# Kernel optimization log

Measured on AMD Instinct MI355X. Metric: run time of the kernel, lower is better.

The kernel has to match this reference:

```python
import jax, jax.numpy as jnp
import numpy as np

IN_F = 256
OUT_F = 64
ALPHA = 0.2  # LeakyReLU negative slope
MASK_VAL = -9e15


def _glorot(key, shape):
    r = np.sqrt(6.0 / (shape[0] + shape[1]))
    return jax.random.uniform(key, shape, jnp.float32, -r, r)


def setup_inputs() -> dict:
    key = jax.random.key(0)
    k_h, k_adj, k_W, k_a = jax.random.split(key, 4)
    B, N = 4, 4096
    h = jax.random.normal(k_h, (B, N, IN_F), jnp.float32)
    adj = jax.random.randint(k_adj, (B, N, N), 0, 2, jnp.int32)
    W = _glorot(k_W, (IN_F, OUT_F))
    a = _glorot(k_a, (2 * OUT_F, 1))
    bias = jnp.zeros((OUT_F,), jnp.float32)
    return {"h": h, "adj": adj, "W": W, "a": a, "bias": bias}


def reference(h, adj, W, a, bias):
    # Wh: [B, N, F_out]
    Wh = jnp.matmul(h, W) + bias
    # additive attention: e_ij = leakyrelu(Wh_i . a1 + Wh_j . a2)
    Wh1 = jnp.matmul(Wh, a[:OUT_F, :])   # [B, N, 1]
    Wh2 = jnp.matmul(Wh, a[OUT_F:, :])   # [B, N, 1]
    e = Wh1 + jnp.swapaxes(Wh2, 2, 1)    # [B, N, N]
    e = jnp.where(e > 0, e, ALPHA * e)   # LeakyReLU
    e = jnp.where(adj > 0, e, MASK_VAL)
    attention = jax.nn.softmax(e, axis=2)
    h_prime = jnp.matmul(attention, Wh)  # [B, N, F_out]
    return jax.nn.elu(h_prime)           # concat=True -> ELU
```

## Files before the change

### kernel.cpp

```cpp
#include <hip/hip_runtime.h>
#include <hip/hip_bf16.h>
#include <cstdint>

#define IN_F 256
#define OUT_F 64
#define NB 4
#define NN 4096
#define ALPHA 0.2f
#define LOG2E 1.4426950408889634f

typedef __attribute__((ext_vector_type(4))) float f32x4;
typedef __attribute__((ext_vector_type(4))) int i32x4;
typedef __attribute__((ext_vector_type(8))) short bf16x8;

static __device__ __forceinline__ ushort f2bf(float x) {
  uint32_t u = __float_as_uint(x);
  uint32_t r = (u + 0x7fffu + ((u >> 16) & 1u)) >> 16;
  return (ushort)r;
}

static __device__ __forceinline__ void gl16(const void* g, void* l) {
  __builtin_amdgcn_global_load_lds(
      (const __attribute__((address_space(1))) void*)g,
      (__attribute__((address_space(3))) void*)l, 16, 0, 0);
}
#define FENCE() asm volatile("" ::: "memory")

__global__ __launch_bounds__(256) void k1_gemm(
    const float* __restrict__ h, const float* __restrict__ W,
    const float* __restrict__ a, const float* __restrict__ bias,
    ushort* __restrict__ WhT, float* __restrict__ Wh1, float* __restrict__ Wh2)
{
  __shared__ float hs[32][33];
  __shared__ float Ws[32][64];
  const int t  = threadIdx.x;
  const int tx = t & 15;
  const int ty = t >> 4;
  const int row0 = blockIdx.x * 32;

  float acc[2][4] = {};

  for (int k0 = 0; k0 < IN_F; k0 += 32) {
    {
      int r = t >> 3, c4 = t & 7;
      *(f32x4*)&hs[r][c4 * 4] =
          *(const f32x4*)(h + (size_t)(row0 + r) * IN_F + k0 + c4 * 4);
    }
    #pragma unroll
    for (int s = 0; s < 2; ++s) {
      int f4 = t + 256 * s;
      int kk = f4 >> 4, c4 = f4 & 15;
      *(f32x4*)&Ws[kk][c4 * 4] = *(const f32x4*)(W + (size_t)(k0 + kk) * OUT_F + c4 * 4);
    }
    __syncthreads();
    #pragma unroll 8
    for (int kk = 0; kk < 32; ++kk) {
      f32x4 bv = *(const f32x4*)&Ws[kk][tx * 4];
      float av0 = hs[ty * 2 + 0][kk];
      float av1 = hs[ty * 2 + 1][kk];
      #pragma unroll
      for (int j = 0; j < 4; ++j) {
        acc[0][j] += av0 * bv[j];
        acc[1][j] += av1 * bv[j];
      }
    }
    __syncthreads();
  }

  #pragma unroll
  for (int i = 0; i < 2; ++i) {
    int row = row0 + ty * 2 + i;
    float s1 = 0.f, s2 = 0.f;
    #pragma unroll
    for (int j = 0; j < 4; ++j) {
      float v = acc[i][j] + bias[tx * 4 + j];
      acc[i][j] = v;
      s1 += v * a[tx * 4 + j];
      s2 += v * a[64 + tx * 4 + j];
    }
    #pragma unroll
    for (int off = 1; off < 16; off <<= 1) {
      s1 += __shfl_xor(s1, off);
      s2 += __shfl_xor(s2, off);
    }
    if (tx == 0) { Wh1[row] = s1 * LOG2E; Wh2[row] = s2 * LOG2E; }
    int bb = row >> 12;
    int n  = row & 4095;
    #pragma unroll
    for (int j = 0; j < 4; ++j) {
      WhT[(((size_t)(bb * OUT_F + tx * 4 + j)) << 12) + n] = f2bf(acc[i][j]);
    }
  }
}

#define NDEPTH 5
#define ADJ_BUF 16384
#define WHT_OFF 81920
#define WHT_BUF 8192
#define WH2_OFF 122880
#define LDS_TOTAL 139264
__global__ __launch_bounds__(512, 1) void k2_attn(
    const int* __restrict__ adj, const ushort* __restrict__ WhT,
    const float* __restrict__ Wh1, const float* __restrict__ Wh2,
    float* __restrict__ out)
{
  extern __shared__ char smem[];
  const int t  = threadIdx.x;
  const int l  = t & 63;
  const int w  = t >> 6;
  const int rq = w >> 1;
  const int kq = w & 1;
  const int g  = l >> 4;
  const int lr = l & 15;
  const int b  = blockIdx.y;
  const int r0 = blockIdx.x << 6;

  const int   rowl = rq * 16 + lr;
  const float wh1  = Wh1[(b << 12) + r0 + rowl];
  asm volatile("" :: "v"(wh1));

  const int*    adjb = adj + ((size_t)b << 24) + ((size_t)r0 << 12);
  const ushort* whb  = WhT + ((size_t)(b * OUT_F) << 12);

  const int*    srcA[4]; int ldsA[4];
  const ushort* srcW[2]; int ldsW[2];
  if (w < 4) {
    #pragma unroll
    for (int i = 0; i < 4; ++i) {
      int e   = ((w * 4 + i) << 6) + l;
      int row = e >> 4;
      int ch  = (e & 15) ^ (row & 7);
      srcA[i] = adjb + (size_t)row * 4096 + (ch << 2);
      ldsA[i] = e << 4;
    }
  } else {
    #pragma unroll
    for (int i = 0; i < 2; ++i) {
      int e    = (((w - 4) * 2 + i) << 6) + l;
      int feat = e >> 3;
      int ch   = (e & 7) ^ (feat & 7);
      srcW[i] = whb + ((size_t)feat << 12) + (ch << 3);
      ldsW[i] = e << 4;
    }
  }

  auto STAGE_A = [&](int s) {
    char* base = smem + (s % NDEPTH) * ADJ_BUF;
    #pragma unroll
    for (int i = 0; i < 4; ++i) gl16(srcA[i] + (s << 6), base + ldsA[i]);
  };
  auto STAGE_W = [&](int s) {
    char* base = smem + WHT_OFF + (s % NDEPTH) * WHT_BUF;
    #pragma unroll
    for (int i = 0; i < 2; ++i) gl16(srcW[i] + (s << 6), base + ldsW[i]);
  };

  f32x4 a0 = {0.f,0.f,0.f,0.f}, a1 = {0.f,0.f,0.f,0.f};
  f32x4 a2 = {0.f,0.f,0.f,0.f}, a3 = {0.f,0.f,0.f,0.f};
  f32x4 as = {0.f,0.f,0.f,0.f};
  bf16x8 ones;
  #pragma unroll
  for (int i = 0; i < 8; ++i) ones[i] = (short)0x3F80;

  const int swzA  = (rowl & 7) << 4;
  const int offA0 = (kq * 128 + g * 32) ^ swzA;
  const int offA1 = (kq * 128 + g * 32 + 16) ^ swzA;
  const int offW  = (kq * 64 + g * 16) ^ ((lr & 7) << 4);

  auto COMPUTE = [&](int s) {
    const char* baseA = smem + (s % NDEPTH) * ADJ_BUF;
    const char* baseW = smem + WHT_OFF + (s % NDEPTH) * WHT_BUF;
    i32x4 ad0 = *(const i32x4*)(baseA + rowl * 256 + offA0);
    i32x4 ad1 = *(const i32x4*)(baseA + rowl * 256 + offA1);
    bf16x8 b0 = *(const bf16x8*)(baseW + (lr     ) * 128 + offW);
    bf16x8 b1 = *(const bf16x8*)(baseW + (lr + 16) * 128 + offW);
    bf16x8 b2 = *(const bf16x8*)(baseW + (lr + 32) * 128 + offW);
    bf16x8 b3 = *(const bf16x8*)(baseW + (lr + 48) * 128 + offW);
    const char* w2b = smem + WH2_OFF + (s << 8) + kq * 128 + g * 32;
    f32x4 w20 = *(const f32x4*)(w2b);
    f32x4 w21 = *(const f32x4*)(w2b + 16);

    float p[8];
    #pragma unroll
    for (int i = 0; i < 8; ++i) {
      float w2 = (i < 4) ? w20[i] : w21[i - 4];
      int   am = (i < 4) ? ad0[i] : ad1[i - 4];
      float s_ = wh1 + w2;
      float lk = fmaf(ALPHA, fminf(s_, 0.f), fmaxf(s_, 0.f));
      float pe = exp2f(lk);
      p[i] = (am > 0) ? pe : 0.0f;
    }
    union { bf16x8 v; uint32_t u[4]; } af;
    #pragma unroll
    for (int i = 0; i < 4; ++i)
      asm("v_cvt_pk_bf16_f32 %0, %1, %2" : "=v"(af.u[i]) : "v"(p[2*i]), "v"(p[2*i+1]));

    as = __builtin_amdgcn_mfma_f32_16x16x32_bf16(af.v, ones, as, 0, 0, 0);
    a0 = __builtin_amdgcn_mfma_f32_16x16x32_bf16(af.v, b0,   a0, 0, 0, 0);
    a1 = __builtin_amdgcn_mfma_f32_16x16x32_bf16(af.v, b1,   a1, 0, 0, 0);
    a2 = __builtin_amdgcn_mfma_f32_16x16x32_bf16(af.v, b2,   a2, 0, 0, 0);
    a3 = __builtin_amdgcn_mfma_f32_16x16x32_bf16(af.v, b3,   a3, 0, 0, 0);
  };

  {
    const float* w2src = Wh2 + (b << 12);
    gl16(w2src + (t << 2),         smem + WH2_OFF + (t << 4));
    gl16(w2src + ((t + 512) << 2), smem + WH2_OFF + 8192 + (t << 4));
  }
  FENCE();
  if (w < 4) { STAGE_A(0); STAGE_A(1); STAGE_A(2); STAGE_A(3); }
  else       { STAGE_W(0); STAGE_W(1); STAGE_W(2); STAGE_W(3); }
  FENCE();

#define WAITB(NA, NW)                                                   \
  do {                                                                  \
    if (w < 4) asm volatile("s_waitcnt vmcnt(" #NA ")" ::: "memory");   \
    else       asm volatile("s_waitcnt vmcnt(" #NW ")" ::: "memory");   \
    __builtin_amdgcn_s_barrier();                                       \
  } while (0)

  for (int s = 0; s < 61; ++s) {
    WAITB(12, 6);
    COMPUTE(s);
    FENCE();
    if (s < 60) { if (w < 4) STAGE_A(s + 4); else STAGE_W(s + 4); }
    FENCE();
  }
  WAITB(8, 4);  COMPUTE(62 - 1);
  WAITB(4, 2);  COMPUTE(62);
  WAITB(0, 0);  COMPUTE(63);
#undef WAITB

  __syncthreads();
  float* sacc = (float*)smem;
  float* ssum = (float*)(smem + 34816);
  #pragma unroll
  for (int r = 0; r < 4; ++r) {
    int rr = rq * 16 + g * 4 + r;
    float* dst = sacc + (kq * 64 + rr) * 68;
    dst[ 0 + lr] = a0[r];
    dst[16 + lr] = a1[r];
    dst[32 + lr] = a2[r];
    dst[48 + lr] = a3[r];
    if (lr == 0) ssum[kq * 64 + rr] = as[r];
  }
  __syncthreads();

  const int row = t >> 3;
  const int c0  = (t & 7) << 3;
  const float* p0 = sacc + row * 68;
  const float* p1 = sacc + (64 + row) * 68;
  float d = ssum[row] + ssum[64 + row];
  float inv = 1.0f / d;
  f32x4 o0, o1;
  #pragma unroll
  for (int j = 0; j < 4; ++j) {
    float x = (p0[c0 + j] + p1[c0 + j]) * inv;
    o0[j] = x > 0.f ? x : expm1f(x);
    float y = (p0[c0 + 4 + j] + p1[c0 + 4 + j]) * inv;
    o1[j] = y > 0.f ? y : expm1f(y);
  }
  size_t ob = ((size_t)((b << 12) + r0 + row) << 6) + c0;
  *(f32x4*)(out + ob)     = o0;
  *(f32x4*)(out + ob + 4) = o1;
}

extern "C" void kernel_launch(void* const* d_in, const int* in_sizes, int n_in,
                              void* d_out, int out_size, void* d_ws, size_t ws_size,
                              hipStream_t stream) {
  const float* h    = (const float*)d_in[0];
  const int*   adj  = (const int*)d_in[1];
  const float* W    = (const float*)d_in[2];
  const float* a    = (const float*)d_in[3];
  const float* bias = (const float*)d_in[4];
  float* out = (float*)d_out;

  char* ws = (char*)d_ws;
  ushort* WhT = (ushort*)ws;
  float*  Wh1 = (float*)(ws + (size_t)NB * OUT_F * NN * 2);
  float*  Wh2 = Wh1 + NB * NN;

  (void)hipFuncSetAttribute((const void*)k2_attn,
                            hipFuncAttributeMaxDynamicSharedMemorySize, LDS_TOTAL);

  k1_gemm<<<dim3(NB * NN / 32), 256, 0, stream>>>(h, W, a, bias, WhT, Wh1, Wh2);
  k2_attn<<<dim3(NN / 64, NB), 512, LDS_TOTAL, stream>>>(adj, WhT, Wh1, Wh2, out);
}
```

Before: 78.91 us.

## Pre-pack adjacency into bitmasks in a separate kernel and stream only WhT

Adds a pre-pass kernel that reads the int32 adjacency matrix once and packs it into 64-bit ballot bitmasks. The attention kernel then loads its 64-row bitmask tile into LDS up front instead of streaming int32 adjacency through a deep pipeline, and pipelines only WhT tiles with depth 4. This cuts LDS use and the adjacency traffic inside the attention kernel. The cost is an extra launch and a full pass over adj in the pack kernel, so total DRAM reads of adj are not reduced.

```diff
diff --git a/kernel.cpp b/kernel.cpp
--- a/kernel.cpp
+++ b/kernel.cpp
@@ -25,6 +25,33 @@
       (__attribute__((address_space(3))) void*)l, 16, 0, 0);
 }
 #define FENCE() asm volatile("" ::: "memory")
+
+__global__ __launch_bounds__(256) void k0_pack(const int* __restrict__ adj,
+                                               unsigned long long* __restrict__ maskp)
+{
+  const int l  = threadIdx.x & 63;
+  const int wv = (blockIdx.x << 2) + (threadIdx.x >> 6);
+  #pragma unroll 2
+  for (int it = 0; it < 32; ++it) {
+    int W    = wv + (it << 13);
+    int c256 = W & 15;
+    int n    = (W >> 4) & 4095;
+    int b    = W >> 16;
+    const int* p = adj + ((size_t)b << 24) + ((size_t)n << 12) + (c256 << 8) + l;
+    int v0 = p[0], v1 = p[64], v2 = p[128], v3 = p[192];
+    unsigned long long m0 = __ballot(v0 != 0);
+    unsigned long long m1 = __ballot(v1 != 0);
+    unsigned long long m2 = __ballot(v2 != 0);
+    unsigned long long m3 = __ballot(v3 != 0);
+    if (l == 0) {
+      size_t base = ((size_t)(b * 64 + c256 * 4) << 12) + n;
+      maskp[base]         = m0;
+      maskp[base + 4096]  = m1;
+      maskp[base + 8192]  = m2;
+      maskp[base + 12288] = m3;
+    }
+  }
+}
 
 __global__ __launch_bounds__(256) void k1_gemm(
     const float* __restrict__ h, const float* __restrict__ W,
@@ -93,14 +120,13 @@
   }
 }
 
-#define NDEPTH 5
-#define ADJ_BUF 16384
-#define WHT_OFF 81920
+#define NDEPTH 4
 #define WHT_BUF 8192
-#define WH2_OFF 122880
-#define LDS_TOTAL 139264
+#define MASK_OFF 32768
+#define WH2_OFF  65536
+#define LDS_TOTAL 81920
 __global__ __launch_bounds__(512, 1) void k2_attn(
-    const int* __restrict__ adj, const ushort* __restrict__ WhT,
+    const unsigned long long* __restrict__ maskp, const ushort* __restrict__ WhT,
     const float* __restrict__ Wh1, const float* __restrict__ Wh2,
     float* __restrict__ out)
 {
@@ -119,40 +145,12 @@
   const float wh1  = Wh1[(b << 12) + r0 + rowl];
   asm volatile("" :: "v"(wh1));
 
-  const int*    adjb = adj + ((size_t)b << 24) + ((size_t)r0 << 12);
-  const ushort* whb  = WhT + ((size_t)(b * OUT_F) << 12);
-
-  const int*    srcA[4]; int ldsA[4];
-  const ushort* srcW[2]; int ldsW[2];
-  if (w < 4) {
-    #pragma unroll
-    for (int i = 0; i < 4; ++i) {
-      int e   = ((w * 4 + i) << 6) + l;
-      int row = e >> 4;
-      int ch  = (e & 15) ^ (row & 7);
-      srcA[i] = adjb + (size_t)row * 4096 + (ch << 2);
-      ldsA[i] = e << 4;
-    }
-  } else {
-    #pragma unroll
-    for (int i = 0; i < 2; ++i) {
-      int e    = (((w - 4) * 2 + i) << 6) + l;
-      int feat = e >> 3;
-      int ch   = (e & 7) ^ (feat & 7);
-      srcW[i] = whb + ((size_t)feat << 12) + (ch << 3);
-      ldsW[i] = e << 4;
-    }
-  }
-
-  auto STAGE_A = [&](int s) {
-    char* base = smem + (s % NDEPTH) * ADJ_BUF;
-    #pragma unroll
-    for (int i = 0; i < 4; ++i) gl16(srcA[i] + (s << 6), base + ldsA[i]);
-  };
+  const ushort* whb = WhT + ((size_t)(b * OUT_F) << 12);
+  const int fW = t >> 3, chW = (t & 7) ^ (fW & 7);
+  const ushort* srcW = whb + ((size_t)fW << 12) + chW * 8;
+  const int ldsW = t << 4;
   auto STAGE_W = [&](int s) {
-    char* base = smem + WHT_OFF + (s % NDEPTH) * WHT_BUF;
-    #pragma unroll
-    for (int i = 0; i < 2; ++i) gl16(srcW[i] + (s << 6), base + ldsW[i]);
+    gl16(srcW + (s << 6), smem + (s & 3) * WHT_BUF + ldsW);
   };
 
   f32x4 a0 = {0.f,0.f,0.f,0.f}, a1 = {0.f,0.f,0.f,0.f};
@@ -162,20 +160,18 @@
   #pragma unroll
   for (int i = 0; i < 8; ++i) ones[i] = (short)0x3F80;
 
-  const int swzA  = (rowl & 7) << 4;
-  const int offA0 = (kq * 128 + g * 32) ^ swzA;
-  const int offA1 = (kq * 128 + g * 32 + 16) ^ swzA;
-  const int offW  = (kq * 64 + g * 16) ^ ((lr & 7) << 4);
+  const int offW = (kq * 64 + g * 16) ^ ((lr & 7) << 4);
+  const int moff = MASK_OFF + rowl * 8 + kq * 4;
+  const int gsh  = g * 8;
 
   auto COMPUTE = [&](int s) {
-    const char* baseA = smem + (s % NDEPTH) * ADJ_BUF;
-    const char* baseW = smem + WHT_OFF + (s % NDEPTH) * WHT_BUF;
-    i32x4 ad0 = *(const i32x4*)(baseA + rowl * 256 + offA0);
-    i32x4 ad1 = *(const i32x4*)(baseA + rowl * 256 + offA1);
+    const char* baseW = smem + (s & 3) * WHT_BUF;
     bf16x8 b0 = *(const bf16x8*)(baseW + (lr     ) * 128 + offW);
     bf16x8 b1 = *(const bf16x8*)(baseW + (lr + 16) * 128 + offW);
     bf16x8 b2 = *(const bf16x8*)(baseW + (lr + 32) * 128 + offW);
     bf16x8 b3 = *(const bf16x8*)(baseW + (lr + 48) * 128 + offW);
+    uint32_t mu  = *(const uint32_t*)(smem + moff + (s << 9));
+    uint32_t mby = (mu >> gsh) & 0xffu;
     const char* w2b = smem + WH2_OFF + (s << 8) + kq * 128 + g * 32;
     f32x4 w20 = *(const f32x4*)(w2b);
     f32x4 w21 = *(const f32x4*)(w2b + 16);
@@ -184,11 +180,10 @@
     #pragma unroll
     for (int i = 0; i < 8; ++i) {
       float w2 = (i < 4) ? w20[i] : w21[i - 4];
-      int   am = (i < 4) ? ad0[i] : ad1[i - 4];
       float s_ = wh1 + w2;
       float lk = fmaf(ALPHA, fminf(s_, 0.f), fmaxf(s_, 0.f));
       float pe = exp2f(lk);
-      p[i] = (am > 0) ? pe : 0.0f;
+      p[i] = (mby & (1u << i)) ? pe : 0.0f;
     }
     union { bf16x8 v; uint32_t u[4]; } af;
     #pragma unroll
@@ -202,34 +197,33 @@
     a3 = __builtin_amdgcn_mfma_f32_16x16x32_bf16(af.v, b3,   a3, 0, 0, 0);
   };
 
+  #pragma unroll
+  for (int i = 0; i < 4; ++i) {
+    int e  = (i << 9) + t;
+    int cb = e >> 5, u = e & 31;
+    const char* src = (const char*)maskp +
+        ((((size_t)(b * 64 + cb)) << 12) + r0) * 8 + u * 16;
+    gl16(src, smem + MASK_OFF + (e << 4));
+  }
   {
     const float* w2src = Wh2 + (b << 12);
     gl16(w2src + (t << 2),         smem + WH2_OFF + (t << 4));
     gl16(w2src + ((t + 512) << 2), smem + WH2_OFF + 8192 + (t << 4));
   }
   FENCE();
-  if (w < 4) { STAGE_A(0); STAGE_A(1); STAGE_A(2); STAGE_A(3); }
-  else       { STAGE_W(0); STAGE_W(1); STAGE_W(2); STAGE_W(3); }
+  STAGE_W(0); STAGE_W(1); STAGE_W(2);
   FENCE();
 
-#define WAITB(NA, NW)                                                   \
-  do {                                                                  \
-    if (w < 4) asm volatile("s_waitcnt vmcnt(" #NA ")" ::: "memory");   \
-    else       asm volatile("s_waitcnt vmcnt(" #NW ")" ::: "memory");   \
-    __builtin_amdgcn_s_barrier();                                       \
-  } while (0)
-
-  for (int s = 0; s < 61; ++s) {
-    WAITB(12, 6);
+  for (int s = 0; s < 64; ++s) {
+    if (s < 62)      asm volatile("s_waitcnt vmcnt(2)" ::: "memory");
+    else if (s == 62) asm volatile("s_waitcnt vmcnt(1)" ::: "memory");
+    else              asm volatile("s_waitcnt vmcnt(0)" ::: "memory");
+    __builtin_amdgcn_s_barrier();
     COMPUTE(s);
     FENCE();
-    if (s < 60) { if (w < 4) STAGE_A(s + 4); else STAGE_W(s + 4); }
+    if (s < 61) STAGE_W(s + 3);
     FENCE();
   }
-  WAITB(8, 4);  COMPUTE(62 - 1);
-  WAITB(4, 2);  COMPUTE(62);
-  WAITB(0, 0);  COMPUTE(63);
-#undef WAITB
 
   __syncthreads();
   float* sacc = (float*)smem;
@@ -279,10 +273,13 @@
   ushort* WhT = (ushort*)ws;
   float*  Wh1 = (float*)(ws + (size_t)NB * OUT_F * NN * 2);
   float*  Wh2 = Wh1 + NB * NN;
+  unsigned long long* maskp =
+      (unsigned long long*)(ws + (size_t)NB * OUT_F * NN * 2 + 2 * NB * NN * 4);
 
   (void)hipFuncSetAttribute((const void*)k2_attn,
                             hipFuncAttributeMaxDynamicSharedMemorySize, LDS_TOTAL);
 
+  k0_pack<<<dim3(2048), 256, 0, stream>>>(adj, maskp);
   k1_gemm<<<dim3(NB * NN / 32), 256, 0, stream>>>(h, W, a, bias, WhT, Wh1, Wh2);
-  k2_attn<<<dim3(NN / 64, NB), 512, LDS_TOTAL, stream>>>(adj, WhT, Wh1, Wh2, out);
-}
+  k2_attn<<<dim3(NN / 64, NB), 512, LDS_TOTAL, stream>>>(maskp, WhT, Wh1, Wh2, out);
+}
```

After: 119.6 us. 1.52x slower.
